# Performance work log

Hardware: AMD Instinct MI355X
Metric: run time of the kernel (lower is better)

## Reference

```python
import jax, jax.numpy as jnp
import numpy as np

EPS = 1e-6  # NAFNet LayerNorm2d eps


def conv1x1(x, W, b):
    # x: [B,C,H,W], W: [O,C], b: [O]
    return jnp.einsum('bchw,oc->bohw', x, W) + b[None, :, None, None]


def layernorm2d(x, w, b):
    # normalize over channel dim (NAFNet LayerNorm2d)
    mu = jnp.mean(x, axis=1, keepdims=True)
    var = jnp.var(x, axis=1, keepdims=True)
    xn = (x - mu) * jax.lax.rsqrt(var + EPS)
    return xn * w[None, :, None, None] + b[None, :, None, None]


def resize_bilinear_ac(x, H, W):
    # bilinear resize with align_corners=True; x: [B,C,h,w] -> [B,C,H,W]
    B, C, h, w = x.shape

    def coords(out, inn):
        s = (inn - 1) / (out - 1)
        c = jnp.arange(out, dtype=jnp.float32) * jnp.float32(s)
        i0 = jnp.clip(jnp.floor(c).astype(jnp.int32), 0, inn - 2)
        f = c - i0.astype(jnp.float32)
        return i0, f

    i0, fy = coords(H, h)
    j0, fx = coords(W, w)
    # rows
    x = x[:, :, i0, :] * (1.0 - fy)[None, None, :, None] + x[:, :, i0 + 1, :] * fy[None, None, :, None]
    # cols
    x = x[:, :, :, j0] * (1.0 - fx)[None, None, None, :] + x[:, :, :, j0 + 1] * fx[None, None, None, :]
    return x


def setup_inputs() -> dict:
    key = jax.random.key(0)
    ks = jax.random.split(key, 24)
    B, c, mem_c, H, W = 8, 128, 64, 128, 128
    h2, w2 = 64, 64
    std = 0.02

    def w2d(k, o, i):
        return jax.random.normal(k, (o, i), dtype=jnp.float32) * np.sqrt(2.0 / o)

    return {
        'x_l': jax.random.normal(ks[0], (B, c, H, W), dtype=jnp.float32),
        'x_r': jax.random.normal(ks[1], (B, mem_c, h2, w2), dtype=jnp.float32),
        'Wm': w2d(ks[2], c, mem_c), 'bm': jnp.zeros((c,), jnp.float32),
        'nl_w': jnp.ones((c,), jnp.float32), 'nl_b': jnp.zeros((c,), jnp.float32),
        'nr_w': jnp.ones((c,), jnp.float32), 'nr_b': jnp.zeros((c,), jnp.float32),
        'Wl1': w2d(ks[3], c, c), 'bl1': jnp.zeros((c,), jnp.float32),
        'Wr1': w2d(ks[4], c, c), 'br1': jnp.zeros((c,), jnp.float32),
        'Wl2': w2d(ks[5], c, c), 'bl2': jnp.zeros((c,), jnp.float32),
        'Wr2': w2d(ks[6], c, c), 'br2': jnp.zeros((c,), jnp.float32),
        'beta': jax.random.normal(ks[7], (1, c, 1, 1), dtype=jnp.float32) * std,
        'gamma': jax.random.normal(ks[8], (1, c, 1, 1), dtype=jnp.float32) * std,
        'Wf': w2d(ks[9], c, 2 * c), 'bf': jnp.zeros((c,), jnp.float32),
    }


def reference(x_l, x_r, Wm, bm, nl_w, nl_b, nr_w, nr_b, Wl1, bl1, Wr1, br1,
              Wl2, bl2, Wr2, br2, beta, gamma, Wf, bf):
    c = x_l.shape[1]
    scale = jnp.float32(c) ** -0.5
    H, W = x_l.shape[-2], x_l.shape[-1]

    x_r = conv1x1(x_r, Wm, bm)
    x_r = resize_bilinear_ac(x_r, H, W)

    Q_l = jnp.transpose(conv1x1(layernorm2d(x_l, nl_w, nl_b), Wl1, bl1), (0, 2, 3, 1))  # b h w c
    Q_r = jnp.transpose(conv1x1(layernorm2d(x_r, nr_w, nr_b), Wr1, br1), (0, 2, 3, 1))  # b h v c
    V_l = jnp.transpose(conv1x1(x_l, Wl2, bl2), (0, 2, 3, 1))  # b h w c
    V_r = jnp.transpose(conv1x1(x_r, Wr2, br2), (0, 2, 3, 1))  # b h v c

    attn = jnp.einsum('bhwc,bhvc->bhwv', Q_l, Q_r) * scale  # [B,H,W,W]
    F_r2l = jnp.einsum('bhwv,bhvc->bhwc', jax.nn.softmax(attn, axis=-1), V_r)
    F_l2r = jnp.einsum('bhwv,bhwc->bhvc', jax.nn.softmax(attn, axis=2), V_l)

    F_r2l = jnp.transpose(F_r2l, (0, 3, 1, 2)) * beta
    F_l2r = jnp.transpose(F_l2r, (0, 3, 1, 2)) * gamma

    x = jnp.concatenate([x_l + F_r2l, x_r + F_l2r], axis=1)
    return conv1x1(x, Wf, bf)
```

## Files before the change

### kernel.cpp

```cpp
#include <hip/hip_runtime.h>
#include <cstdint>
#include <cstddef>

typedef __attribute__((ext_vector_type(8))) short short8;
typedef __attribute__((ext_vector_type(4))) float f32x4;

#define MFMA16(a,b,c) __builtin_amdgcn_mfma_f32_16x16x32_bf16((a),(b),(c),0,0,0)

static __device__ __forceinline__ float bf2f(unsigned short u){
    unsigned int x = ((unsigned int)u) << 16;
    return __builtin_bit_cast(float, x);
}
static __device__ __forceinline__ unsigned short f2bf(float f){
    unsigned int x = __builtin_bit_cast(unsigned int, f);
    x = x + 0x7FFFu + ((x >> 16) & 1u);
    return (unsigned short)(x >> 16);
}


__global__ void k_prep(const float* __restrict__ Wl1, const float* __restrict__ bl1,
                       const float* __restrict__ Wr1, const float* __restrict__ br1,
                       const float* __restrict__ Wl2, const float* __restrict__ Wr2,
                       const float* __restrict__ Wf,
                       const float* __restrict__ nlw, const float* __restrict__ nlb,
                       const float* __restrict__ nrw, const float* __restrict__ nrb,
                       unsigned short* __restrict__ wl1e, unsigned short* __restrict__ wr1e,
                       unsigned short* __restrict__ wl2b, unsigned short* __restrict__ wr2b,
                       unsigned short* __restrict__ wf1b, unsigned short* __restrict__ wf2b,
                       float* __restrict__ S1l, float* __restrict__ S1r,
                       float* __restrict__ beffl, float* __restrict__ beffr)
{
    int o = blockIdx.x;
    int c = threadIdx.x;
    float wl = Wl1[o*128+c] * nlw[c];
    unsigned short wlb = f2bf(wl);
    wl1e[o*128+c] = wlb;
    float wr = Wr1[o*128+c] * nrw[c];
    unsigned short wrb = f2bf(wr);
    wr1e[o*128+c] = wrb;
    wl2b[o*128+c] = f2bf(Wl2[o*128+c]);
    wr2b[o*128+c] = f2bf(Wr2[o*128+c]);
    wf1b[o*128+c] = f2bf(Wf[o*256+c]);
    wf2b[o*128+c] = f2bf(Wf[o*256+128+c]);

    __shared__ float red[4][128];
    red[0][c] = bf2f(wlb);
    red[1][c] = Wl1[o*128+c]*nlb[c];
    red[2][c] = bf2f(wrb);
    red[3][c] = Wr1[o*128+c]*nrb[c];
    __syncthreads();
    if (c < 4) {
        float s = 0.f;
        for (int i = 0; i < 128; i++) s += red[c][i];
        if      (c == 0) S1l[o]   = s;
        else if (c == 1) beffl[o] = bl1[o] + s;
        else if (c == 2) S1r[o]   = s;
        else             beffr[o] = br1[o] + s;
    }
}

__global__ void k_memconv(const float* __restrict__ xr, const float* __restrict__ Wm,
                          const float* __restrict__ bm, unsigned short* __restrict__ R0n)
{
    __shared__ float Xs[64][65];
    __shared__ float Ws[128][65];
    int blk = blockIdx.x;
    int b  = blk >> 6;
    int p0 = (blk & 63) * 64;
    int t = threadIdx.x;
    for (int k = 0; k < 16; k++) {
        int idx = t + 256*k;
        int c = idx >> 6, pi = idx & 63;
        Xs[c][pi] = xr[((long)b*64 + c)*4096 + p0 + pi];
    }
    for (int k = 0; k < 32; k++) {
        int idx = t + 256*k;
        int o = idx >> 6, c = idx & 63;
        Ws[o][c] = Wm[o*64 + c];
    }
    __syncthreads();
    int og = t >> 3, pg = t & 7;
    int o0 = og*4, pp0 = pg*8;
    float acc[4][8];
    #pragma unroll
    for (int j = 0; j < 4; j++)
        #pragma unroll
        for (int k = 0; k < 8; k++) acc[j][k] = bm[o0+j];
    for (int c = 0; c < 64; c++) {
        float xv[8], wv[4];
        #pragma unroll
        for (int k = 0; k < 8; k++) xv[k] = Xs[c][pp0+k];
        #pragma unroll
        for (int j = 0; j < 4; j++) wv[j] = Ws[o0+j][c];
        #pragma unroll
        for (int j = 0; j < 4; j++)
            #pragma unroll
            for (int k = 0; k < 8; k++) acc[j][k] += wv[j]*xv[k];
    }
    #pragma unroll
    for (int j = 0; j < 4; j++)
        #pragma unroll
        for (int k = 0; k < 8; k++)
            R0n[((long)b*4096 + p0 + pp0 + k)*128 + o0 + j] = f2bf(acc[j][k]);
}

__global__ void k_upsample(const unsigned short* __restrict__ R0n,
                           unsigned short* __restrict__ XR)
{
    int t = threadIdx.x;
    int c = t & 127;
    long pix = (long)blockIdx.x * 2 + (t >> 7);
    int b = (int)(pix >> 14);
    int rem = (int)(pix & 16383);
    int Y = rem >> 7, X = rem & 127;
    const float s = 63.0f / 127.0f;
    float cy = Y * s, cx = X * s;
    int y0 = min((int)floorf(cy), 62);
    int x0 = min((int)floorf(cx), 62);
    float fy = cy - (float)y0, fx = cx - (float)x0;
    const unsigned short* base = R0n + ((long)b*4096)*128;
    float v00 = bf2f(base[(y0*64 + x0    )*128 + c]);
    float v01 = bf2f(base[(y0*64 + x0 + 1)*128 + c]);
    float v10 = bf2f(base[((y0+1)*64 + x0    )*128 + c]);
    float v11 = bf2f(base[((y0+1)*64 + x0 + 1)*128 + c]);
    float r0 = v00*(1.f-fy) + v10*fy;
    float r1 = v01*(1.f-fy) + v11*fy;
    XR[pix*128 + c] = f2bf(r0*(1.f-fx) + r1*fx);
}

__global__ void k_transpose(const float* __restrict__ xl, unsigned short* __restrict__ XL)
{
    __shared__ float tile[32][33];
    int blk = blockIdx.x;
    int pt = blk & 511;
    int ct = (blk >> 9) & 3;
    int b  = blk >> 11;
    int p0 = pt*32, c0 = ct*32;
    int t = threadIdx.x;
    const float* src = xl + (long)b*128*16384;
    #pragma unroll
    for (int k = 0; k < 4; k++) {
        int idx = t + 256*k;
        int ci = idx >> 5, pi = idx & 31;
        tile[ci][pi] = src[(long)(c0+ci)*16384 + p0 + pi];
    }
    __syncthreads();
    unsigned short* dst = XL + (long)b*16384*128;
    #pragma unroll
    for (int k = 0; k < 4; k++) {
        int idx = t + 256*k;
        int pi = idx >> 5, ci = idx & 31;
        dst[(long)(p0+pi)*128 + c0 + ci] = f2bf(tile[ci][pi]);
    }
}

__global__ void k_stats(const unsigned short* __restrict__ X,
                        float* __restrict__ mu, float* __restrict__ rs, int npix)
{
    int t = threadIdx.x;
    int lane = t & 63, wv = t >> 6;
    long pix = (long)blockIdx.x*4 + wv;
    if (pix >= npix) return;
    const unsigned short* row = X + pix*128;
    unsigned int pr = *(const unsigned int*)(row + lane*2);
    float a = bf2f((unsigned short)(pr & 0xFFFFu));
    float b = bf2f((unsigned short)(pr >> 16));
    float s = a + b, s2 = a*a + b*b;
    #pragma unroll
    for (int d = 1; d < 64; d <<= 1) { s += __shfl_xor(s, d); s2 += __shfl_xor(s2, d); }
    if (lane == 0) {
        float m = s * (1.0f/128.0f);
        float var = s2 * (1.0f/128.0f) - m*m;
        mu[pix] = m;
        rs[pix] = rsqrtf(var + 1e-6f);
    }
}

#define LDQ 136
constexpr int K4_LDS = 4*128*LDQ*2 + (13*128 + 8*128 + 256)*4;

__global__ __launch_bounds__(512) void k_scam(
    const unsigned short* __restrict__ XL, const unsigned short* __restrict__ XR,
    const unsigned short* __restrict__ wl1e, const unsigned short* __restrict__ wr1e,
    const unsigned short* __restrict__ wl2b, const unsigned short* __restrict__ wr2b,
    const unsigned short* __restrict__ wf1b, const unsigned short* __restrict__ wf2b,
    const float* __restrict__ muL, const float* __restrict__ rsL,
    const float* __restrict__ muR, const float* __restrict__ rsR,
    const float* __restrict__ S1l, const float* __restrict__ S1r,
    const float* __restrict__ beffl, const float* __restrict__ beffr,
    const float* __restrict__ bl2, const float* __restrict__ br2,
    const float* __restrict__ beta, const float* __restrict__ gam,
    const float* __restrict__ bfv, float* __restrict__ out)
{
    extern __shared__ char smem[];
    unsigned short* bufA  = (unsigned short*)smem;
    unsigned short* bufB  = bufA  + 128*LDQ;
    unsigned short* bufVL = bufB  + 128*LDQ;
    unsigned short* bufVR = bufVL + 128*LDQ;
    float* vecs    = (float*)(bufVR + 128*LDQ);
    float* colpart = vecs + 13*128;
    float* colred  = colpart + 8*128;

    int tid = threadIdx.x;
    int lane = tid & 63, wv = tid >> 6;
    int l16 = lane & 15, lg = lane >> 4;
    int bh = blockIdx.x;
    int b = bh >> 7, h = bh & 127;
    long pixbase = (long)b*16384 + (long)h*128;
    const unsigned short* Abl = XL + pixbase*128;
    const unsigned short* Abr = XR + pixbase*128;

    if (tid < 128) {
        vecs[0*128+tid]  = muL[pixbase + tid];
        vecs[1*128+tid]  = rsL[pixbase + tid];
        vecs[2*128+tid]  = muR[pixbase + tid];
        vecs[3*128+tid]  = rsR[pixbase + tid];
        vecs[4*128+tid]  = S1l[tid];
        vecs[5*128+tid]  = beffl[tid];
        vecs[6*128+tid]  = S1r[tid];
        vecs[7*128+tid]  = beffr[tid];
        vecs[8*128+tid]  = bl2[tid];
        vecs[9*128+tid]  = br2[tid];
        vecs[10*128+tid] = beta[tid];
        vecs[11*128+tid] = gam[tid];
        vecs[12*128+tid] = bfv[tid];
    }
    __syncthreads();

    int p0 = wv * 16;

    f32x4 acc[8];
    auto conv = [&](const unsigned short* Asrc, const unsigned short* Wsrc){
        #pragma unroll
        for (int t = 0; t < 8; t++) acc[t] = (f32x4){0.f,0.f,0.f,0.f};
        #pragma unroll
        for (int kc = 0; kc < 4; kc++) {
            short8 a = *(const short8*)(Asrc + (p0+l16)*128 + kc*32 + lg*8);
            #pragma unroll
            for (int t = 0; t < 8; t++) {
                short8 bw = *(const short8*)(Wsrc + (t*16+l16)*128 + kc*32 + lg*8);
                acc[t] = MFMA16(a, bw, acc[t]);
            }
        }
    };
    auto epiQ = [&](const float* vmu, const float* vrs, const float* vS1,
                    const float* vbe, unsigned short* dst){
        #pragma unroll
        for (int r = 0; r < 4; r++) {
            int p = p0 + lg*4 + r;
            float mu = vmu[p], rs = vrs[p];
            #pragma unroll
            for (int t = 0; t < 8; t++) {
                int o = t*16 + l16;
                dst[p*LDQ + o] = f2bf(rs*(acc[t][r] - mu*vS1[o]) + vbe[o]);
            }
        }
    };
    auto epiV = [&](const float* vb, unsigned short* dst){
        #pragma unroll
        for (int t = 0; t < 8; t++) {
            int o = t*16 + l16;
            float bias = vb[o];
            #pragma unroll
            for (int r = 0; r < 4; r++) {
                int p = p0 + lg*4 + r;
                dst[o*LDQ + p] = f2bf(acc[t][r] + bias);
            }
        }
    };

    conv(Abl, wl1e); epiQ(vecs+0*128, vecs+1*128, vecs+4*128, vecs+5*128, bufA);
    conv(Abr, wr1e); epiQ(vecs+2*128, vecs+3*128, vecs+6*128, vecs+7*128, bufB);
    conv(Abl, wl2b); epiV(vecs+8*128, bufVL);
    conv(Abr, wr2b); epiV(vecs+9*128, bufVR);
    __syncthreads();

    int w0 = p0;
    f32x4 s[8];
    #pragma unroll
    for (int t = 0; t < 8; t++) s[t] = (f32x4){0.f,0.f,0.f,0.f};
    #pragma unroll
    for (int kc = 0; kc < 4; kc++) {
        short8 a = *(const short8*)(bufA + (w0+l16)*LDQ + kc*32 + lg*8);
        #pragma unroll
        for (int t = 0; t < 8; t++) {
            short8 bq = *(const short8*)(bufB + (t*16+l16)*LDQ + kc*32 + lg*8);
            s[t] = MFMA16(a, bq, s[t]);
        }
    }
    const float scale = 0.08838834764831845f;
    #pragma unroll
    for (int t = 0; t < 8; t++)
        #pragma unroll
        for (int r = 0; r < 4; r++) s[t][r] *= scale;

    float rm[4];
    #pragma unroll
    for (int r = 0; r < 4; r++) {
        float m = s[0][r];
        #pragma unroll
        for (int t = 1; t < 8; t++) m = fmaxf(m, s[t][r]);
        #pragma unroll
        for (int d = 1; d < 16; d <<= 1) m = fmaxf(m, __shfl_xor(m, d));
        rm[r] = m;
    }
    #pragma unroll
    for (int t = 0; t < 8; t++) {
        float m = fmaxf(fmaxf(s[t][0], s[t][1]), fmaxf(s[t][2], s[t][3]));
        m = fmaxf(m, __shfl_xor(m, 16));
        m = fmaxf(m, __shfl_xor(m, 32));
        if (lane < 16) colpart[wv*128 + t*16 + lane] = m;
    }
    __syncthreads();
    if (tid < 128) {
        float m = colpart[tid];
        for (int i = 1; i < 8; i++) m = fmaxf(m, colpart[i*128 + tid]);
        colred[tid] = m;
    }
    __syncthreads();

    float rsum[4];
    #pragma unroll
    for (int r = 0; r < 4; r++) {
        float a = 0.f;
        #pragma unroll
        for (int t = 0; t < 8; t++) { float e = __expf(s[t][r] - rm[r]); s[t][r] = e; a += e; }
        #pragma unroll
        for (int d = 1; d < 16; d <<= 1) a += __shfl_xor(a, d);
        rsum[r] = a;
    }
    #pragma unroll
    for (int t = 0; t < 8; t++) {
        #pragma unroll
        for (int r = 0; r < 4; r++) {
            bufA[(w0 + lg*4 + r)*LDQ + t*16 + l16] = f2bf(s[t][r] / rsum[r]);
        }
    }
    #pragma unroll
    for (int t = 0; t < 8; t++) {
        float cmax = colred[t*16 + l16];
        float a = 0.f;
        #pragma unroll
        for (int r = 0; r < 4; r++) {
            float e2 = s[t][r] * __expf(rm[r] - cmax);
            s[t][r] = e2; a += e2;
        }
        a += __shfl_xor(a, 16);
        a += __shfl_xor(a, 32);
        if (lane < 16) colpart[wv*128 + t*16 + lane] = a;
    }
    __syncthreads();
    if (tid < 128) {
        float sm = 0.f;
        for (int i = 0; i < 8; i++) sm += colpart[i*128 + tid];
        colred[128 + tid] = sm;
    }
    __syncthreads();
    #pragma unroll
    for (int t = 0; t < 8; t++) {
        float inv = 1.0f / colred[128 + t*16 + l16];
        #pragma unroll
        for (int r = 0; r < 4; r++) {
            bufB[(t*16 + l16)*LDQ + w0 + lg*4 + r] = f2bf(s[t][r] * inv);
        }
    }
    __syncthreads();

    f32x4 f1[8], f2[8];
    #pragma unroll
    for (int t = 0; t < 8; t++) { f1[t] = (f32x4){0.f,0.f,0.f,0.f}; f2[t] = (f32x4){0.f,0.f,0.f,0.f}; }
    #pragma unroll
    for (int kc = 0; kc < 4; kc++) {
        short8 a1 = *(const short8*)(bufA + (w0+l16)*LDQ + kc*32 + lg*8);
        short8 a2 = *(const short8*)(bufB + (w0+l16)*LDQ + kc*32 + lg*8);
        #pragma unroll
        for (int t = 0; t < 8; t++) {
            short8 bv1 = *(const short8*)(bufVR + (t*16+l16)*LDQ + kc*32 + lg*8);
            f1[t] = MFMA16(a1, bv1, f1[t]);
            short8 bv2 = *(const short8*)(bufVL + (t*16+l16)*LDQ + kc*32 + lg*8);
            f2[t] = MFMA16(a2, bv2, f2[t]);
        }
    }
    __syncthreads();

    #pragma unroll
    for (int t = 0; t < 8; t++) {
        int c = t*16 + l16;
        float bet = vecs[10*128 + c], gm = vecs[11*128 + c];
        #pragma unroll
        for (int r = 0; r < 4; r++) {
            int p = w0 + lg*4 + r;
            float xl = bf2f(Abl[p*128 + c]);
            bufA[p*LDQ + c] = f2bf(xl + bet*f1[t][r]);
            float xr = bf2f(Abr[p*128 + c]);
            bufB[p*LDQ + c] = f2bf(xr + gm*f2[t][r]);
        }
    }
    __syncthreads();

    int o0 = wv * 16;
    f32x4 oacc[8];
    #pragma unroll
    for (int t = 0; t < 8; t++) oacc[t] = (f32x4){0.f,0.f,0.f,0.f};
    #pragma unroll
    for (int kc = 0; kc < 4; kc++) {
        short8 aw1 = *(const short8*)(wf1b + (o0+l16)*128 + kc*32 + lg*8);
        short8 aw2 = *(const short8*)(wf2b + (o0+l16)*128 + kc*32 + lg*8);
        #pragma unroll
        for (int t = 0; t < 8; t++) {
            short8 b1 = *(const short8*)(bufA + (t*16+l16)*LDQ + kc*32 + lg*8);
            oacc[t] = MFMA16(aw1, b1, oacc[t]);
            short8 b2 = *(const short8*)(bufB + (t*16+l16)*LDQ + kc*32 + lg*8);
            oacc[t] = MFMA16(aw2, b2, oacc[t]);
        }
    }
    float* outb = out + (long)b*2097152 + (long)h*128;
    #pragma unroll
    for (int t = 0; t < 8; t++) {
        #pragma unroll
        for (int r = 0; r < 4; r++) {
            int o = o0 + lg*4 + r;
            outb[(long)o*16384 + t*16 + l16] = oacc[t][r] + vecs[12*128 + o];
        }
    }
}

extern "C" void kernel_launch(void* const* d_in, const int* in_sizes, int n_in,
                              void* d_out, int out_size, void* d_ws, size_t ws_size,
                              hipStream_t stream)
{
    const float* x_l = (const float*)d_in[0];
    const float* x_r = (const float*)d_in[1];
    const float* Wm  = (const float*)d_in[2];
    const float* bm  = (const float*)d_in[3];
    const float* nlw = (const float*)d_in[4];
    const float* nlb = (const float*)d_in[5];
    const float* nrw = (const float*)d_in[6];
    const float* nrb = (const float*)d_in[7];
    const float* Wl1 = (const float*)d_in[8];
    const float* bl1 = (const float*)d_in[9];
    const float* Wr1 = (const float*)d_in[10];
    const float* br1 = (const float*)d_in[11];
    const float* Wl2 = (const float*)d_in[12];
    const float* bl2 = (const float*)d_in[13];
    const float* Wr2 = (const float*)d_in[14];
    const float* br2 = (const float*)d_in[15];
    const float* beta = (const float*)d_in[16];
    const float* gam  = (const float*)d_in[17];
    const float* Wf   = (const float*)d_in[18];
    const float* bf   = (const float*)d_in[19];
    float* out = (float*)d_out;

    char* ws = (char*)d_ws;
    size_t off = 0;
    auto alloc = [&](size_t bytes) -> void* {
        void* p = ws + off;
        off += (bytes + 255) & ~(size_t)255;
        return p;
    };
    unsigned short* XL   = (unsigned short*)alloc((size_t)16777216*2);
    unsigned short* XR   = (unsigned short*)alloc((size_t)16777216*2);
    unsigned short* R0n  = (unsigned short*)alloc((size_t)4194304*2);
    float* muL = (float*)alloc((size_t)131072*4);
    float* rsL = (float*)alloc((size_t)131072*4);
    float* muR = (float*)alloc((size_t)131072*4);
    float* rsR = (float*)alloc((size_t)131072*4);
    unsigned short* wl1e = (unsigned short*)alloc((size_t)16384*2);
    unsigned short* wr1e = (unsigned short*)alloc((size_t)16384*2);
    unsigned short* wl2b = (unsigned short*)alloc((size_t)16384*2);
    unsigned short* wr2b = (unsigned short*)alloc((size_t)16384*2);
    unsigned short* wf1b = (unsigned short*)alloc((size_t)16384*2);
    unsigned short* wf2b = (unsigned short*)alloc((size_t)16384*2);
    float* S1l   = (float*)alloc(128*4);
    float* S1r   = (float*)alloc(128*4);
    float* beffl = (float*)alloc(128*4);
    float* beffr = (float*)alloc(128*4);

    (void)in_sizes; (void)n_in; (void)out_size; (void)ws_size;

    hipFuncSetAttribute((const void*)k_scam,
                        hipFuncAttributeMaxDynamicSharedMemorySize, K4_LDS);

    k_prep<<<128, 128, 0, stream>>>(Wl1, bl1, Wr1, br1, Wl2, Wr2, Wf,
                                    nlw, nlb, nrw, nrb,
                                    wl1e, wr1e, wl2b, wr2b, wf1b, wf2b,
                                    S1l, S1r, beffl, beffr);
    k_memconv<<<512, 256, 0, stream>>>(x_r, Wm, bm, R0n);
    k_upsample<<<65536, 256, 0, stream>>>(R0n, XR);
    k_transpose<<<16384, 256, 0, stream>>>(x_l, XL);
    k_stats<<<32768, 256, 0, stream>>>(XL, muL, rsL, 131072);
    k_stats<<<32768, 256, 0, stream>>>(XR, muR, rsR, 131072);
    k_scam<<<1024, 512, K4_LDS, stream>>>(XL, XR, wl1e, wr1e, wl2b, wr2b,
                                          wf1b, wf2b, muL, rsL, muR, rsR,
                                          S1l, S1r, beffl, beffr,
                                          bl2, br2, beta, gam, bf, out);
}
```

Before: 446.8 us.

## Fuse layernorm stats into transpose/upsample and split attention kernel across 16 waves

Fold the per-pixel mean/rstd computation into the upsample and x_l transpose kernels, which removes the two separate stats launches and their re-reads of XL/XR. The main attention kernel now runs 1024 threads instead of 512, with each wave handling half the columns. Row and column softmax reductions are rebuilt with cross-half shared-memory exchanges. The x_l/x_r residual tiles are staged into LDS before the final conv. The prep kernel's reduction now uses warp shuffles. The trade-offs are higher register pressure from the 1024-thread launch bound and more barriers.

```diff
diff --git a/kernel.cpp b/kernel.cpp
--- a/kernel.cpp
+++ b/kernel.cpp
@@ -49,13 +49,15 @@
     red[2][c] = bf2f(wrb);
     red[3][c] = Wr1[o*128+c]*nrb[c];
     __syncthreads();
-    if (c < 4) {
-        float s = 0.f;
-        for (int i = 0; i < 128; i++) s += red[c][i];
-        if      (c == 0) S1l[o]   = s;
-        else if (c == 1) beffl[o] = bl1[o] + s;
-        else if (c == 2) S1r[o]   = s;
-        else             beffr[o] = br1[o] + s;
+    int g = c >> 5, j = c & 31;
+    float sv = red[g][j] + red[g][j+32] + red[g][j+64] + red[g][j+96];
+    #pragma unroll
+    for (int d = 1; d < 32; d <<= 1) sv += __shfl_xor(sv, d);
+    if (j == 0) {
+        if      (g == 0) S1l[o]   = sv;
+        else if (g == 1) beffl[o] = bl1[o] + sv;
+        else if (g == 2) S1r[o]   = sv;
+        else             beffr[o] = br1[o] + sv;
     }
 }
 
@@ -104,17 +106,20 @@
             R0n[((long)b*4096 + p0 + pp0 + k)*128 + o0 + j] = f2bf(acc[j][k]);
 }
 
-__global__ void k_upsample(const unsigned short* __restrict__ R0n,
-                           unsigned short* __restrict__ XR)
+__global__ void k_xr(const unsigned short* __restrict__ R0n,
+                     unsigned short* __restrict__ XR,
+                     float* __restrict__ muR, float* __restrict__ rsR)
 {
+    __shared__ float part[2][2][2];
     int t = threadIdx.x;
     int c = t & 127;
-    long pix = (long)blockIdx.x * 2 + (t >> 7);
+    int pl = t >> 7;
+    long pix = (long)blockIdx.x * 2 + pl;
     int b = (int)(pix >> 14);
     int rem = (int)(pix & 16383);
     int Y = rem >> 7, X = rem & 127;
-    const float s = 63.0f / 127.0f;
-    float cy = Y * s, cx = X * s;
+    const float sc = 63.0f / 127.0f;
+    float cy = Y * sc, cx = X * sc;
     int y0 = min((int)floorf(cy), 62);
     int x0 = min((int)floorf(cx), 62);
     float fy = cy - (float)y0, fx = cx - (float)x0;
@@ -125,61 +130,69 @@
     float v11 = bf2f(base[((y0+1)*64 + x0 + 1)*128 + c]);
     float r0 = v00*(1.f-fy) + v10*fy;
     float r1 = v01*(1.f-fy) + v11*fy;
-    XR[pix*128 + c] = f2bf(r0*(1.f-fx) + r1*fx);
-}
-
-__global__ void k_transpose(const float* __restrict__ xl, unsigned short* __restrict__ XL)
+    float val = r0*(1.f-fx) + r1*fx;
+    XR[pix*128 + c] = f2bf(val);
+    float sv = val, s2 = val*val;
+    #pragma unroll
+    for (int d = 1; d < 64; d <<= 1) { sv += __shfl_xor(sv, d); s2 += __shfl_xor(s2, d); }
+    int wh = (t >> 6) & 1;
+    if ((t & 63) == 0) { part[pl][wh][0] = sv; part[pl][wh][1] = s2; }
+    __syncthreads();
+    if ((t & 127) == 0) {
+        float S  = part[pl][0][0] + part[pl][1][0];
+        float S2 = part[pl][0][1] + part[pl][1][1];
+        float m = S * (1.0f/128.0f);
+        float var = S2 * (1.0f/128.0f) - m*m;
+        muR[pix] = m;
+        rsR[pix] = rsqrtf(var + 1e-6f);
+    }
+}
+
+__global__ void k_xl(const float* __restrict__ xl, unsigned short* __restrict__ XL,
+                     float* __restrict__ muL, float* __restrict__ rsL)
 {
-    __shared__ float tile[32][33];
+    __shared__ float tile[128][33];
+    __shared__ float partS[8][32];
+    __shared__ float partS2[8][32];
     int blk = blockIdx.x;
-    int pt = blk & 511;
-    int ct = (blk >> 9) & 3;
-    int b  = blk >> 11;
-    int p0 = pt*32, c0 = ct*32;
+    int b  = blk >> 9;
+    int p0 = (blk & 511) * 32;
+    const float* src = xl + (long)b*128*16384;
     int t = threadIdx.x;
-    const float* src = xl + (long)b*128*16384;
-    #pragma unroll
-    for (int k = 0; k < 4; k++) {
+    #pragma unroll
+    for (int k = 0; k < 16; k++) {
         int idx = t + 256*k;
-        int ci = idx >> 5, pi = idx & 31;
-        tile[ci][pi] = src[(long)(c0+ci)*16384 + p0 + pi];
-    }
-    __syncthreads();
-    unsigned short* dst = XL + (long)b*16384*128;
-    #pragma unroll
-    for (int k = 0; k < 4; k++) {
-        int idx = t + 256*k;
-        int pi = idx >> 5, ci = idx & 31;
-        dst[(long)(p0+pi)*128 + c0 + ci] = f2bf(tile[ci][pi]);
-    }
-}
-
-__global__ void k_stats(const unsigned short* __restrict__ X,
-                        float* __restrict__ mu, float* __restrict__ rs, int npix)
-{
-    int t = threadIdx.x;
-    int lane = t & 63, wv = t >> 6;
-    long pix = (long)blockIdx.x*4 + wv;
-    if (pix >= npix) return;
-    const unsigned short* row = X + pix*128;
-    unsigned int pr = *(const unsigned int*)(row + lane*2);
-    float a = bf2f((unsigned short)(pr & 0xFFFFu));
-    float b = bf2f((unsigned short)(pr >> 16));
-    float s = a + b, s2 = a*a + b*b;
-    #pragma unroll
-    for (int d = 1; d < 64; d <<= 1) { s += __shfl_xor(s, d); s2 += __shfl_xor(s2, d); }
-    if (lane == 0) {
-        float m = s * (1.0f/128.0f);
-        float var = s2 * (1.0f/128.0f) - m*m;
-        mu[pix] = m;
-        rs[pix] = rsqrtf(var + 1e-6f);
+        int cc = idx >> 5, pi = idx & 31;
+        tile[cc][pi] = src[(long)cc*16384 + p0 + pi];
+    }
+    __syncthreads();
+    unsigned short* dst = XL + ((long)b*16384 + p0)*128;
+    int cw = t & 127, ph = t >> 7;
+    #pragma unroll
+    for (int k = 0; k < 16; k++) {
+        int pi = ph*16 + k;
+        dst[(long)pi*128 + cw] = f2bf(tile[cw][pi]);
+    }
+    int sub = t >> 5, pj = t & 31;
+    float sv = 0.f, s2 = 0.f;
+    #pragma unroll
+    for (int j = 0; j < 16; j++) { float v = tile[sub*16+j][pj]; sv += v; s2 += v*v; }
+    partS[sub][pj] = sv; partS2[sub][pj] = s2;
+    __syncthreads();
+    if (t < 32) {
+        float S = 0.f, S2 = 0.f;
+        #pragma unroll
+        for (int i = 0; i < 8; i++) { S += partS[i][t]; S2 += partS2[i][t]; }
+        float m = S*(1.0f/128.0f), var = S2*(1.0f/128.0f) - m*m;
+        muL[(long)b*16384 + p0 + t] = m;
+        rsL[(long)b*16384 + p0 + t] = rsqrtf(var + 1e-6f);
     }
 }
 
 #define LDQ 136
-constexpr int K4_LDS = 4*128*LDQ*2 + (13*128 + 8*128 + 256)*4;
-
-__global__ __launch_bounds__(512) void k_scam(
+constexpr int K4_LDS = 4*128*LDQ*2 + (13*128 + 8*128 + 8*128 + 2*128 + 2*128)*4;
+
+__global__ __launch_bounds__(1024) void k_scam(
     const unsigned short* __restrict__ XL, const unsigned short* __restrict__ XR,
     const unsigned short* __restrict__ wl1e, const unsigned short* __restrict__ wr1e,
     const unsigned short* __restrict__ wl2b, const unsigned short* __restrict__ wr2b,
@@ -197,13 +210,18 @@
     unsigned short* bufB  = bufA  + 128*LDQ;
     unsigned short* bufVL = bufB  + 128*LDQ;
     unsigned short* bufVR = bufVL + 128*LDQ;
-    float* vecs    = (float*)(bufVR + 128*LDQ);
-    float* colpart = vecs + 13*128;
-    float* colred  = colpart + 8*128;
+    float* vecs     = (float*)(bufVR + 128*LDQ);
+    float* colpart  = vecs + 13*128;
+    float* colpart2 = colpart + 8*128;
+    float* rowmax   = colpart2 + 8*128;
+    float* rowsum   = rowmax + 2*128;
 
     int tid = threadIdx.x;
     int lane = tid & 63, wv = tid >> 6;
     int l16 = lane & 15, lg = lane >> 4;
+    int rw = wv & 7, half = wv >> 3;
+    int p0 = rw * 16;
+    int th = half * 4;
     int bh = blockIdx.x;
     int b = bh >> 7, h = bh & 127;
     long pixbase = (long)b*16384 + (long)h*128;
@@ -227,44 +245,43 @@
     }
     __syncthreads();
 
-    int p0 = wv * 16;
-
-    f32x4 acc[8];
+    f32x4 acc[4];
     auto conv = [&](const unsigned short* Asrc, const unsigned short* Wsrc){
         #pragma unroll
-        for (int t = 0; t < 8; t++) acc[t] = (f32x4){0.f,0.f,0.f,0.f};
+        for (int t4 = 0; t4 < 4; t4++) acc[t4] = (f32x4){0.f,0.f,0.f,0.f};
         #pragma unroll
         for (int kc = 0; kc < 4; kc++) {
             short8 a = *(const short8*)(Asrc + (p0+l16)*128 + kc*32 + lg*8);
             #pragma unroll
-            for (int t = 0; t < 8; t++) {
-                short8 bw = *(const short8*)(Wsrc + (t*16+l16)*128 + kc*32 + lg*8);
-                acc[t] = MFMA16(a, bw, acc[t]);
+            for (int t4 = 0; t4 < 4; t4++) {
+                int tt = th + t4;
+                short8 bw = *(const short8*)(Wsrc + (tt*16+l16)*128 + kc*32 + lg*8);
+                acc[t4] = MFMA16(a, bw, acc[t4]);
             }
         }
     };
     auto epiQ = [&](const float* vmu, const float* vrs, const float* vS1,
-                    const float* vbe, unsigned short* dst){
+                    const float* vbe, unsigned short* dstb){
         #pragma unroll
         for (int r = 0; r < 4; r++) {
             int p = p0 + lg*4 + r;
             float mu = vmu[p], rs = vrs[p];
             #pragma unroll
-            for (int t = 0; t < 8; t++) {
-                int o = t*16 + l16;
-                dst[p*LDQ + o] = f2bf(rs*(acc[t][r] - mu*vS1[o]) + vbe[o]);
+            for (int t4 = 0; t4 < 4; t4++) {
+                int o = (th+t4)*16 + l16;
+                dstb[p*LDQ + o] = f2bf(rs*(acc[t4][r] - mu*vS1[o]) + vbe[o]);
             }
         }
     };
-    auto epiV = [&](const float* vb, unsigned short* dst){
-        #pragma unroll
-        for (int t = 0; t < 8; t++) {
-            int o = t*16 + l16;
+    auto epiV = [&](const float* vb, unsigned short* dstb){
+        #pragma unroll
+        for (int t4 = 0; t4 < 4; t4++) {
+            int o = (th+t4)*16 + l16;
             float bias = vb[o];
             #pragma unroll
             for (int r = 0; r < 4; r++) {
                 int p = p0 + lg*4 + r;
-                dst[o*LDQ + p] = f2bf(acc[t][r] + bias);
+                dstb[o*LDQ + p] = f2bf(acc[t4][r] + bias);
             }
         }
     };
@@ -275,152 +292,180 @@
     conv(Abr, wr2b); epiV(vecs+9*128, bufVR);
     __syncthreads();
 
-    int w0 = p0;
-    f32x4 s[8];
-    #pragma unroll
-    for (int t = 0; t < 8; t++) s[t] = (f32x4){0.f,0.f,0.f,0.f};
+    f32x4 s[4];
+    #pragma unroll
+    for (int t4 = 0; t4 < 4; t4++) s[t4] = (f32x4){0.f,0.f,0.f,0.f};
     #pragma unroll
     for (int kc = 0; kc < 4; kc++) {
-        short8 a = *(const short8*)(bufA + (w0+l16)*LDQ + kc*32 + lg*8);
-        #pragma unroll
-        for (int t = 0; t < 8; t++) {
-            short8 bq = *(const short8*)(bufB + (t*16+l16)*LDQ + kc*32 + lg*8);
-            s[t] = MFMA16(a, bq, s[t]);
+        short8 a = *(const short8*)(bufA + (p0+l16)*LDQ + kc*32 + lg*8);
+        #pragma unroll
+        for (int t4 = 0; t4 < 4; t4++) {
+            short8 bq = *(const short8*)(bufB + ((th+t4)*16+l16)*LDQ + kc*32 + lg*8);
+            s[t4] = MFMA16(a, bq, s[t4]);
         }
     }
     const float scale = 0.08838834764831845f;
     #pragma unroll
-    for (int t = 0; t < 8; t++)
-        #pragma unroll
-        for (int r = 0; r < 4; r++) s[t][r] *= scale;
+    for (int t4 = 0; t4 < 4; t4++)
+        #pragma unroll
+        for (int r = 0; r < 4; r++) s[t4][r] *= scale;
 
     float rm[4];
     #pragma unroll
     for (int r = 0; r < 4; r++) {
-        float m = s[0][r];
-        #pragma unroll
-        for (int t = 1; t < 8; t++) m = fmaxf(m, s[t][r]);
+        float m = fmaxf(fmaxf(s[0][r], s[1][r]), fmaxf(s[2][r], s[3][r]));
         #pragma unroll
         for (int d = 1; d < 16; d <<= 1) m = fmaxf(m, __shfl_xor(m, d));
         rm[r] = m;
     }
-    #pragma unroll
-    for (int t = 0; t < 8; t++) {
-        float m = fmaxf(fmaxf(s[t][0], s[t][1]), fmaxf(s[t][2], s[t][3]));
+    if (l16 == 0) {
+        #pragma unroll
+        for (int r = 0; r < 4; r++) rowmax[half*128 + p0 + lg*4 + r] = rm[r];
+    }
+    #pragma unroll
+    for (int t4 = 0; t4 < 4; t4++) {
+        float m = fmaxf(fmaxf(s[t4][0], s[t4][1]), fmaxf(s[t4][2], s[t4][3]));
         m = fmaxf(m, __shfl_xor(m, 16));
         m = fmaxf(m, __shfl_xor(m, 32));
-        if (lane < 16) colpart[wv*128 + t*16 + lane] = m;
-    }
-    __syncthreads();
-    if (tid < 128) {
-        float m = colpart[tid];
-        for (int i = 1; i < 8; i++) m = fmaxf(m, colpart[i*128 + tid]);
-        colred[tid] = m;
-    }
-    __syncthreads();
-
-    float rsum[4];
+        if (lane < 16) colpart[rw*128 + (th+t4)*16 + lane] = m;
+    }
+    __syncthreads();
+
     #pragma unroll
     for (int r = 0; r < 4; r++) {
+        int row = p0 + lg*4 + r;
+        rm[r] = fmaxf(rowmax[row], rowmax[128 + row]);
+    }
+    float cmax[4];
+    #pragma unroll
+    for (int t4 = 0; t4 < 4; t4++) {
+        int col = (th+t4)*16 + l16;
+        float m = colpart[col];
+        #pragma unroll
+        for (int i = 1; i < 8; i++) m = fmaxf(m, colpart[i*128 + col]);
+        cmax[t4] = m;
+    }
+
+    float rsumP[4] = {0.f,0.f,0.f,0.f};
+    #pragma unroll
+    for (int t4 = 0; t4 < 4; t4++)
+        #pragma unroll
+        for (int r = 0; r < 4; r++) {
+            float e = __expf(s[t4][r] - rm[r]);
+            s[t4][r] = e; rsumP[r] += e;
+        }
+    #pragma unroll
+    for (int r = 0; r < 4; r++) {
+        float a = rsumP[r];
+        #pragma unroll
+        for (int d = 1; d < 16; d <<= 1) a += __shfl_xor(a, d);
+        rsumP[r] = a;
+    }
+    if (l16 == 0) {
+        #pragma unroll
+        for (int r = 0; r < 4; r++) rowsum[half*128 + p0 + lg*4 + r] = rsumP[r];
+    }
+    #pragma unroll
+    for (int t4 = 0; t4 < 4; t4++) {
         float a = 0.f;
         #pragma unroll
-        for (int t = 0; t < 8; t++) { float e = __expf(s[t][r] - rm[r]); s[t][r] = e; a += e; }
-        #pragma unroll
-        for (int d = 1; d < 16; d <<= 1) a += __shfl_xor(a, d);
-        rsum[r] = a;
-    }
-    #pragma unroll
-    for (int t = 0; t < 8; t++) {
-        #pragma unroll
-        for (int r = 0; r < 4; r++) {
-            bufA[(w0 + lg*4 + r)*LDQ + t*16 + l16] = f2bf(s[t][r] / rsum[r]);
-        }
-    }
-    #pragma unroll
-    for (int t = 0; t < 8; t++) {
-        float cmax = colred[t*16 + l16];
-        float a = 0.f;
-        #pragma unroll
-        for (int r = 0; r < 4; r++) {
-            float e2 = s[t][r] * __expf(rm[r] - cmax);
-            s[t][r] = e2; a += e2;
-        }
+        for (int r = 0; r < 4; r++) a += s[t4][r] * __expf(rm[r] - cmax[t4]);
         a += __shfl_xor(a, 16);
         a += __shfl_xor(a, 32);
-        if (lane < 16) colpart[wv*128 + t*16 + lane] = a;
-    }
-    __syncthreads();
-    if (tid < 128) {
-        float sm = 0.f;
-        for (int i = 0; i < 8; i++) sm += colpart[i*128 + tid];
-        colred[128 + tid] = sm;
-    }
-    __syncthreads();
-    #pragma unroll
-    for (int t = 0; t < 8; t++) {
-        float inv = 1.0f / colred[128 + t*16 + l16];
+        if (lane < 16) colpart2[rw*128 + (th+t4)*16 + lane] = a;
+    }
+    __syncthreads();
+
+    float rsum[4];
+    #pragma unroll
+    for (int r = 0; r < 4; r++) {
+        int row = p0 + lg*4 + r;
+        rsum[r] = rowsum[row] + rowsum[128 + row];
+    }
+    #pragma unroll
+    for (int t4 = 0; t4 < 4; t4++)
+        #pragma unroll
+        for (int r = 0; r < 4; r++)
+            bufA[(p0 + lg*4 + r)*LDQ + (th+t4)*16 + l16] = f2bf(s[t4][r] / rsum[r]);
+
+    #pragma unroll
+    for (int t4 = 0; t4 < 4; t4++) {
+        #pragma unroll
+        for (int r = 0; r < 4; r++) s[t4][r] *= __expf(rm[r] - cmax[t4]);
+        int col = (th+t4)*16 + l16;
+        float cs = 0.f;
+        #pragma unroll
+        for (int i = 0; i < 8; i++) cs += colpart2[i*128 + col];
+        float inv = 1.0f / cs;
+        #pragma unroll
+        for (int r = 0; r < 4; r++)
+            bufB[col*LDQ + p0 + lg*4 + r] = f2bf(s[t4][r] * inv);
+    }
+    __syncthreads();
+
+    f32x4 f1[4], f2[4];
+    #pragma unroll
+    for (int t4 = 0; t4 < 4; t4++) { f1[t4] = (f32x4){0.f,0.f,0.f,0.f}; f2[t4] = (f32x4){0.f,0.f,0.f,0.f}; }
+    #pragma unroll
+    for (int kc = 0; kc < 4; kc++) {
+        short8 a1 = *(const short8*)(bufA + (p0+l16)*LDQ + kc*32 + lg*8);
+        short8 a2 = *(const short8*)(bufB + (p0+l16)*LDQ + kc*32 + lg*8);
+        #pragma unroll
+        for (int t4 = 0; t4 < 4; t4++) {
+            short8 bv1 = *(const short8*)(bufVR + ((th+t4)*16+l16)*LDQ + kc*32 + lg*8);
+            f1[t4] = MFMA16(a1, bv1, f1[t4]);
+            short8 bv2 = *(const short8*)(bufVL + ((th+t4)*16+l16)*LDQ + kc*32 + lg*8);
+            f2[t4] = MFMA16(a2, bv2, f2[t4]);
+        }
+    }
+    __syncthreads();
+
+    #pragma unroll
+    for (int k = 0; k < 2; k++) {
+        int idx = tid + 1024*k;
+        int p = idx >> 4, cg = idx & 15;
+        *(short8*)(bufVL + p*LDQ + cg*8) = *(const short8*)(Abl + p*128 + cg*8);
+        *(short8*)(bufVR + p*LDQ + cg*8) = *(const short8*)(Abr + p*128 + cg*8);
+    }
+    __syncthreads();
+
+    #pragma unroll
+    for (int t4 = 0; t4 < 4; t4++) {
+        int c = (th+t4)*16 + l16;
+        float bet = vecs[10*128 + c], gm = vecs[11*128 + c];
         #pragma unroll
         for (int r = 0; r < 4; r++) {
-            bufB[(t*16 + l16)*LDQ + w0 + lg*4 + r] = f2bf(s[t][r] * inv);
-        }
-    }
-    __syncthreads();
-
-    f32x4 f1[8], f2[8];
-    #pragma unroll
-    for (int t = 0; t < 8; t++) { f1[t] = (f32x4){0.f,0.f,0.f,0.f}; f2[t] = (f32x4){0.f,0.f,0.f,0.f}; }
+            int p = p0 + lg*4 + r;
+            float xlv = bf2f(bufVL[p*LDQ + c]);
+            bufA[p*LDQ + c] = f2bf(xlv + bet*f1[t4][r]);
+            float xrv = bf2f(bufVR[p*LDQ + c]);
+            bufB[p*LDQ + c] = f2bf(xrv + gm*f2[t4][r]);
+        }
+    }
+    __syncthreads();
+
+    f32x4 oacc[4];
+    #pragma unroll
+    for (int t4 = 0; t4 < 4; t4++) oacc[t4] = (f32x4){0.f,0.f,0.f,0.f};
     #pragma unroll
     for (int kc = 0; kc < 4; kc++) {
-        short8 a1 = *(const short8*)(bufA + (w0+l16)*LDQ + kc*32 + lg*8);
-        short8 a2 = *(const short8*)(bufB + (w0+l16)*LDQ + kc*32 + lg*8);
-        #pragma unroll
-        for (int t = 0; t < 8; t++) {
-            short8 bv1 = *(const short8*)(bufVR + (t*16+l16)*LDQ + kc*32 + lg*8);
-            f1[t] = MFMA16(a1, bv1, f1[t]);
-            short8 bv2 = *(const short8*)(bufVL + (t*16+l16)*LDQ + kc*32 + lg*8);
-            f2[t] = MFMA16(a2, bv2, f2[t]);
-        }
-    }
-    __syncthreads();
-
-    #pragma unroll
-    for (int t = 0; t < 8; t++) {
-        int c = t*16 + l16;
-        float bet = vecs[10*128 + c], gm = vecs[11*128 + c];
+        short8 aw1 = *(const short8*)(wf1b + (p0+l16)*128 + kc*32 + lg*8);
+        short8 aw2 = *(const short8*)(wf2b + (p0+l16)*128 + kc*32 + lg*8);
+        #pragma unroll
+        for (int t4 = 0; t4 < 4; t4++) {
+            short8 b1 = *(const short8*)(bufA + ((th+t4)*16+l16)*LDQ + kc*32 + lg*8);
+            oacc[t4] = MFMA16(aw1, b1, oacc[t4]);
+            short8 b2 = *(const short8*)(bufB + ((th+t4)*16+l16)*LDQ + kc*32 + lg*8);
+            oacc[t4] = MFMA16(aw2, b2, oacc[t4]);
+        }
+    }
+    float* outb = out + (long)b*2097152 + (long)h*128;
+    #pragma unroll
+    for (int t4 = 0; t4 < 4; t4++) {
         #pragma unroll
         for (int r = 0; r < 4; r++) {
-            int p = w0 + lg*4 + r;
-            float xl = bf2f(Abl[p*128 + c]);
-            bufA[p*LDQ + c] = f2bf(xl + bet*f1[t][r]);
-            float xr = bf2f(Abr[p*128 + c]);
-            bufB[p*LDQ + c] = f2bf(xr + gm*f2[t][r]);
-        }
-    }
-    __syncthreads();
-
-    int o0 = wv * 16;
-    f32x4 oacc[8];
-    #pragma unroll
-    for (int t = 0; t < 8; t++) oacc[t] = (f32x4){0.f,0.f,0.f,0.f};
-    #pragma unroll
-    for (int kc = 0; kc < 4; kc++) {
-        short8 aw1 = *(const short8*)(wf1b + (o0+l16)*128 + kc*32 + lg*8);
-        short8 aw2 = *(const short8*)(wf2b + (o0+l16)*128 + kc*32 + lg*8);
-        #pragma unroll
-        for (int t = 0; t < 8; t++) {
-            short8 b1 = *(const short8*)(bufA + (t*16+l16)*LDQ + kc*32 + lg*8);
-            oacc[t] = MFMA16(aw1, b1, oacc[t]);
-            short8 b2 = *(const short8*)(bufB + (t*16+l16)*LDQ + kc*32 + lg*8);
-            oacc[t] = MFMA16(aw2, b2, oacc[t]);
-        }
-    }
-    float* outb = out + (long)b*2097152 + (long)h*128;
-    #pragma unroll
-    for (int t = 0; t < 8; t++) {
-        #pragma unroll
-        for (int r = 0; r < 4; r++) {
-            int o = o0 + lg*4 + r;
-            outb[(long)o*16384 + t*16 + l16] = oacc[t][r] + vecs[12*128 + o];
+            int o = p0 + lg*4 + r;
+            outb[(long)o*16384 + (th+t4)*16 + l16] = oacc[t4][r] + vecs[12*128 + o];
         }
     }
 }
@@ -486,12 +531,10 @@
                                     wl1e, wr1e, wl2b, wr2b, wf1b, wf2b,
                                     S1l, S1r, beffl, beffr);
     k_memconv<<<512, 256, 0, stream>>>(x_r, Wm, bm, R0n);
-    k_upsample<<<65536, 256, 0, stream>>>(R0n, XR);
-    k_transpose<<<16384, 256, 0, stream>>>(x_l, XL);
-    k_stats<<<32768, 256, 0, stream>>>(XL, muL, rsL, 131072);
-    k_stats<<<32768, 256, 0, stream>>>(XR, muR, rsR, 131072);
-    k_scam<<<1024, 512, K4_LDS, stream>>>(XL, XR, wl1e, wr1e, wl2b, wr2b,
-                                          wf1b, wf2b, muL, rsL, muR, rsR,
-                                          S1l, S1r, beffl, beffr,
-                                          bl2, br2, beta, gam, bf, out);
-}
+    k_xr<<<65536, 256, 0, stream>>>(R0n, XR, muR, rsR);
+    k_xl<<<4096, 256, 0, stream>>>(x_l, XL, muL, rsL);
+    k_scam<<<1024, 1024, K4_LDS, stream>>>(XL, XR, wl1e, wr1e, wl2b, wr2b,
+                                           wf1b, wf2b, muL, rsL, muR, rsR,
+                                           S1l, S1r, beffl, beffr,
+                                           bl2, br2, beta, gam, bf, out);
+}
```

Result: faster. 419.8 us (-6.0%).
